# Performance work log

Hardware: AMD Instinct MI355X
Metric: run time of the kernel (lower is better)

Reference implementation:

```python
import jax, jax.numpy as jnp
import numpy as np

D_MODEL = 1024
N_HEADS = 16
HEAD_DIM = D_MODEL // N_HEADS
BATCH = 4
SEQ = 2048


def setup_inputs() -> dict:
    key = jax.random.key(0)
    k_x, k_wqkv, k_bqkv, k_wo, k_bo = jax.random.split(key, 5)
    x = jax.random.normal(k_x, (BATCH, SEQ, D_MODEL), dtype=jnp.float32)
    # causal mask: True = masked (upper triangle, excluding diagonal)
    mask = jnp.triu(jnp.ones((SEQ, SEQ), dtype=bool), k=1)
    lim = 1.0 / np.sqrt(D_MODEL)
    w_qkv = jax.random.uniform(k_wqkv, (D_MODEL, 3 * D_MODEL), jnp.float32, -lim, lim)
    b_qkv = jax.random.uniform(k_bqkv, (3 * D_MODEL,), jnp.float32, -lim, lim)
    w_out = jax.random.uniform(k_wo, (D_MODEL, D_MODEL), jnp.float32, -lim, lim)
    b_out = jax.random.uniform(k_bo, (D_MODEL,), jnp.float32, -lim, lim)
    return {"x": x, "mask": mask, "w_qkv": w_qkv, "b_qkv": b_qkv,
            "w_out": w_out, "b_out": b_out}


def reference(x, mask, w_qkv, b_qkv, w_out, b_out):
    b, s, _ = x.shape
    scale = HEAD_DIM ** -0.5
    qkv = x @ w_qkv + b_qkv                          # [b, s, 3*d]
    qkv = qkv.reshape(b, s, 3, N_HEADS, HEAD_DIM)
    qkv = jnp.transpose(qkv, (2, 0, 3, 1, 4))        # [3, b, h, s, hd]
    q, k, v = qkv[0], qkv[1], qkv[2]
    attn = jnp.einsum('bhqd,bhkd->bhqk', q, k) * scale
    attn = jnp.where(mask, -jnp.inf, attn)
    attn = jax.nn.softmax(attn, axis=-1)
    out = jnp.einsum('bhqk,bhkd->bhqd', attn, v)     # [b, h, s, hd]
    out = jnp.transpose(out, (0, 2, 1, 3)).reshape(b, s, D_MODEL)
    return out @ w_out + b_out
```

## Files before the change

### kernel.cpp

```cpp
#include <hip/hip_runtime.h>
#include <stdint.h>

typedef unsigned short u16;
typedef __attribute__((ext_vector_type(8))) short short8;
typedef __attribute__((ext_vector_type(4))) float f32x4;
typedef __attribute__((ext_vector_type(16))) float f32x16;

#define DEV static __device__ __forceinline__

#define QSCALE 0.18033688011112042f

DEV float fast_exp2(float x) { return __builtin_amdgcn_exp2f(x); }

DEV float bf2f(u16 u) { union { uint32_t i; float f; } x; x.i = ((uint32_t)u) << 16; return x.f; }
DEV u16 f2bf(float f) {
  union { float f; uint32_t i; } x; x.f = f;
  uint32_t r = x.i + 0x7FFFu + ((x.i >> 16) & 1u);
  return (u16)(r >> 16);
}
DEV uint32_t pk_bf16(float lo, float hi) {
  uint32_t r;
  asm("v_cvt_pk_bf16_f32 %0, %1, %2" : "=v"(r) : "v"(lo), "v"(hi));
  return r;
}

DEV void async_copy16(void* lds_dst, const void* gsrc) {
  typedef __attribute__((address_space(1))) void* gp_t;
  typedef __attribute__((address_space(3))) void* lp_t;
  __builtin_amdgcn_global_load_lds((gp_t)(uintptr_t)gsrc,
                                   (lp_t)(uint32_t)(uintptr_t)lds_dst, 16, 0, 0);
}

DEV void gemm_bt_core(const u16* __restrict__ A, const u16* __restrict__ Bt, int K,
                      int m0, int n0, uint8_t* As, uint8_t* Bs,
                      f32x4 (&acc)[4][4], int wave, int lane, int wm, int wn) {
#pragma unroll
  for (int mt = 0; mt < 4; ++mt)
#pragma unroll
    for (int nt = 0; nt < 4; ++nt)
      acc[mt][nt] = (f32x4){0.f, 0.f, 0.f, 0.f};

  for (int k0 = 0; k0 < K; k0 += 64) {
    __syncthreads();
#pragma unroll
    for (int i = 0; i < 4; ++i) {
      int cb = wave * 256 + i * 64;
      int c  = cb + lane;
      int r  = c >> 3;
      int ks = (c & 7) ^ (r & 7);
      async_copy16(As + cb * 16 + lane * 16, A  + (size_t)(m0 + r) * K + k0 + ks * 8);
      async_copy16(Bs + cb * 16 + lane * 16, Bt + (size_t)(n0 + r) * K + k0 + ks * 8);
    }
    __syncthreads();

    short8 af[2][4], bf_[2][4];
#pragma unroll
    for (int kk = 0; kk < 2; ++kk)
#pragma unroll
      for (int t = 0; t < 4; ++t) {
        int ra = wm + t * 16 + (lane & 15);
        af[kk][t]  = *(const short8*)(As + ra * 128 + (((kk * 4 + (lane >> 4)) ^ (ra & 7)) << 4));
        int rb = wn + t * 16 + (lane & 15);
        bf_[kk][t] = *(const short8*)(Bs + rb * 128 + (((kk * 4 + (lane >> 4)) ^ (rb & 7)) << 4));
      }
#pragma unroll
    for (int kk = 0; kk < 2; ++kk)
#pragma unroll
      for (int mt = 0; mt < 4; ++mt)
#pragma unroll
        for (int nt = 0; nt < 4; ++nt)
          acc[mt][nt] = __builtin_amdgcn_mfma_f32_16x16x32_bf16(af[kk][mt], bf_[kk][nt],
                                                                acc[mt][nt], 0, 0, 0);
  }
}

#define BUF_BYTES 49152

DEV void stage_slot(const u16* __restrict__ A, const u16* __restrict__ Bt,
                    int m0, int n0, int k0, uint8_t* buf, int tid) {
  uint8_t* As = buf;
  uint8_t* Bs = buf + 32768;
#pragma unroll
  for (int i = 0; i < 4; ++i) {
    int c = i * 512 + tid;
    int r = c >> 3;
    int ks = (c & 7) ^ (r & 7);
    async_copy16(As + c * 16, A + (size_t)(m0 + r) * 1024 + k0 + ks * 8);
  }
#pragma unroll
  for (int i = 0; i < 2; ++i) {
    int c = i * 512 + tid;
    int r = c >> 3;
    int ks = (c & 7) ^ (r & 7);
    async_copy16(Bs + c * 16, Bt + (size_t)(n0 + r) * 1024 + k0 + ks * 8);
  }
}

DEV void gemm256_core(const u16* __restrict__ A, const u16* __restrict__ Bt,
                      int m0, int n0, uint8_t* lds,
                      f32x4 (&acc)[4][4], int wave, int lane, int tid) {
  const int wm = (wave >> 1) * 64, wn = (wave & 1) * 64;
#pragma unroll
  for (int mf = 0; mf < 4; ++mf)
#pragma unroll
    for (int nf = 0; nf < 4; ++nf)
      acc[mf][nf] = (f32x4){0.f, 0.f, 0.f, 0.f};

  stage_slot(A, Bt, m0, n0, 0,  lds,             tid);
  stage_slot(A, Bt, m0, n0, 64, lds + BUF_BYTES, tid);
  asm volatile("s_waitcnt vmcnt(6)" ::: "memory");
  __builtin_amdgcn_s_barrier();

#pragma unroll 1
  for (int kt = 0; kt < 16; ++kt) {
    const uint8_t* Ab = lds + (kt & 1) * BUF_BYTES;
    const uint8_t* Bb = Ab + 32768;

    short8 a0[4], b0[4], a1[4], b1[4];
#pragma unroll
    for (int f = 0; f < 4; ++f) {
      int ra = wm + f * 16 + (lane & 15);
      int rb = wn + f * 16 + (lane & 15);
      a0[f] = *(const short8*)(Ab + ra * 128 + (((lane >> 4) ^ (ra & 7)) << 4));
      b0[f] = *(const short8*)(Bb + rb * 128 + (((lane >> 4) ^ (rb & 7)) << 4));
    }
#pragma unroll
    for (int f = 0; f < 4; ++f) {
      int ra = wm + f * 16 + (lane & 15);
      int rb = wn + f * 16 + (lane & 15);
      a1[f] = *(const short8*)(Ab + ra * 128 + (((4 + (lane >> 4)) ^ (ra & 7)) << 4));
      b1[f] = *(const short8*)(Bb + rb * 128 + (((4 + (lane >> 4)) ^ (rb & 7)) << 4));
    }

    asm volatile("s_waitcnt lgkmcnt(8)" ::: "memory");
    __builtin_amdgcn_sched_barrier(0);
    __builtin_amdgcn_s_setprio(1);
#pragma unroll
    for (int mf = 0; mf < 4; ++mf)
#pragma unroll
      for (int nf = 0; nf < 4; ++nf)
        acc[mf][nf] = __builtin_amdgcn_mfma_f32_16x16x32_bf16(a0[mf], b0[nf],
                                                              acc[mf][nf], 0, 0, 0);
    __builtin_amdgcn_s_setprio(0);

    asm volatile("s_waitcnt lgkmcnt(0)" ::: "memory");
    __builtin_amdgcn_sched_barrier(0);
    __builtin_amdgcn_s_barrier();

    if (kt + 2 < 16)
      stage_slot(A, Bt, m0, n0, (kt + 2) * 64, lds + (kt & 1) * BUF_BYTES, tid);

    __builtin_amdgcn_s_setprio(1);
#pragma unroll
    for (int mf = 0; mf < 4; ++mf)
#pragma unroll
      for (int nf = 0; nf < 4; ++nf)
        acc[mf][nf] = __builtin_amdgcn_mfma_f32_16x16x32_bf16(a1[mf], b1[nf],
                                                              acc[mf][nf], 0, 0, 0);
    __builtin_amdgcn_s_setprio(0);

    if (kt + 2 < 16) asm volatile("s_waitcnt vmcnt(6)" ::: "memory");
    else             asm volatile("s_waitcnt vmcnt(0)" ::: "memory");
    __builtin_amdgcn_s_barrier();
  }
}

__global__ __launch_bounds__(256, 2) void k_gemm_qkv(
    const u16* __restrict__ X, const u16* __restrict__ WT, const float* __restrict__ bias,
    u16* __restrict__ Q, u16* __restrict__ Kv, u16* __restrict__ Vt) {
  __shared__ __attribute__((aligned(16))) uint8_t As[16384];
  __shared__ __attribute__((aligned(16))) uint8_t Bs[16384];
  const int lane = threadIdx.x & 63, wave = threadIdx.x >> 6;
  const int wm = (wave >> 1) * 64, wn = (wave & 1) * 64;
  const int m0 = blockIdx.x * 128, n0 = blockIdx.y * 128;
  f32x4 acc[4][4];
  gemm_bt_core(X, WT, 1024, m0, n0, As, Bs, acc, wave, lane, wm, wn);
#pragma unroll
  for (int nt = 0; nt < 4; ++nt) {
    int n = n0 + wn + nt * 16 + (lane & 15);
    float bv = bias[n];
    int which = n >> 10, h = (n >> 6) & 15, hd = n & 63;
    if (which == 2) {
#pragma unroll
      for (int mt = 0; mt < 4; ++mt) {
        int m = m0 + wm + mt * 16 + (lane >> 4) * 4;
        int b = m >> 11, s = m & 2047;
        u16 tmp[4];
#pragma unroll
        for (int rg = 0; rg < 4; ++rg) tmp[rg] = f2bf(acc[mt][nt][rg] + bv);
        *(uint64_t*)(Vt + ((size_t)(b * 16 + h) * 64 + hd) * 2048 + s) = *(const uint64_t*)tmp;
      }
    } else {
      u16* base = (which == 0) ? Q : Kv;
      const float mul = (which == 0) ? QSCALE : 1.0f;
#pragma unroll
      for (int mt = 0; mt < 4; ++mt)
#pragma unroll
        for (int rg = 0; rg < 4; ++rg) {
          int m = m0 + wm + mt * 16 + (lane >> 4) * 4 + rg;
          int b = m >> 11, s = m & 2047;
          base[((size_t)(b * 16 + h) * 2048 + s) * 64 + hd] = f2bf((acc[mt][nt][rg] + bv) * mul);
        }
    }
  }
}

__global__ __launch_bounds__(512, 2) void k_gemm_out(
    const u16* __restrict__ A, const u16* __restrict__ WT, const float* __restrict__ bias,
    float* __restrict__ Out) {
  __shared__ __attribute__((aligned(16))) uint8_t lds[2 * BUF_BYTES];
  const int tid = threadIdx.x, lane = tid & 63, wave = tid >> 6;
  const int wm = (wave >> 1) * 64, wn = (wave & 1) * 64;
  const int m0 = blockIdx.x * 256, n0 = blockIdx.y * 128;
  f32x4 acc[4][4];
  gemm256_core(A, WT, m0, n0, lds, acc, wave, lane, tid);
#pragma unroll
  for (int nf = 0; nf < 4; ++nf) {
    int n = n0 + wn + nf * 16 + (lane & 15);
    float bv = bias[n];
#pragma unroll
    for (int mf = 0; mf < 4; ++mf)
#pragma unroll
      for (int rg = 0; rg < 4; ++rg) {
        int m = m0 + wm + mf * 16 + (lane >> 4) * 4 + rg;
        Out[(size_t)m * 1024 + n] = acc[mf][nf][rg] + bv;
      }
  }
}

__global__ __launch_bounds__(256) void k_cvt_x(const float* __restrict__ src,
                                               u16* __restrict__ dst, int n8) {
  int i = blockIdx.x * 256 + threadIdx.x;
  if (i >= n8) return;
  float4 a = *(const float4*)(src + (size_t)i * 8);
  float4 b = *(const float4*)(src + (size_t)i * 8 + 4);
  u16 tmp[8] = {f2bf(a.x), f2bf(a.y), f2bf(a.z), f2bf(a.w),
                f2bf(b.x), f2bf(b.y), f2bf(b.z), f2bf(b.w)};
  *(short8*)(dst + (size_t)i * 8) = *(const short8*)tmp;
}

__global__ __launch_bounds__(256) void k_transpose_f32(
    const float* __restrict__ src, u16* __restrict__ dst, int R, int C) {
  __shared__ u16 tile[64][72];
  const int tr = blockIdx.x * 64, tc = blockIdx.y * 64;
  for (int c = threadIdx.x; c < 1024; c += 256) {
    int r = c >> 4, c4 = (c & 15) * 4;
    float4 v = *(const float4*)(src + (size_t)(tr + r) * C + tc + c4);
    tile[r][c4 + 0] = f2bf(v.x); tile[r][c4 + 1] = f2bf(v.y);
    tile[r][c4 + 2] = f2bf(v.z); tile[r][c4 + 3] = f2bf(v.w);
  }
  __syncthreads();
  for (int c = threadIdx.x; c < 512; c += 256) {
    int oc = c >> 3, r8 = (c & 7) * 8;
    u16 tmp[8];
#pragma unroll
    for (int i = 0; i < 8; ++i) tmp[i] = tile[r8 + i][oc];
    *(short8*)(dst + (size_t)(tc + oc) * R + tr + r8) = *(const short8*)tmp;
  }
}

DEV void stage_tile(const u16* __restrict__ Kg, const u16* __restrict__ Vg,
                    uint8_t* kb, uint8_t* vb, int t, int tid) {
#pragma unroll
  for (int i = 0; i < 2; ++i) {
    int c = i * 256 + tid;
    int r = c >> 3;
    int ks = (c & 7) ^ (r & 7);
    async_copy16(kb + c * 16, Kg + (size_t)(t * 64 + r) * 64 + ks * 8);
    async_copy16(vb + c * 16, Vg + (size_t)r * 2048 + t * 64 + ks * 8);
  }
}

__global__ __launch_bounds__(256, 2) void k_attn(
    const u16* __restrict__ Q, const u16* __restrict__ K,
    const u16* __restrict__ Vt, u16* __restrict__ O) {
  __shared__ __attribute__((aligned(16))) uint8_t kbuf[2][8192];
  __shared__ __attribute__((aligned(16))) uint8_t vbuf[2][8192];
  const int tid = threadIdx.x;
  const int lane = tid & 63;
  const int wave = tid >> 6;
  const int q32 = lane & 31, hv = lane >> 5;
  const float NEG_INF = -__builtin_inff();

  int L = blockIdx.x;
  int bh = (L & 7) * 8 + ((L >> 3) >> 3);
  int pair = (L >> 3) & 7;
  const int b = bh >> 4, h = bh & 15;
  const size_t hb = (size_t)bh * (2048 * 64);
  const u16* Qg = Q + hb;
  const u16* Kg = K + hb;
  const u16* Vg = Vt + hb;

#pragma unroll 1
  for (int which = 0; which < 2; ++which) {
    const int s = which ? (15 - pair) : pair;
    const int nt = 2 * (s + 1);
    const int qbase = s * 128 + wave * 32;
    const int qg = qbase + q32;
    const int my_nt = ((qbase + 31) >> 6) + 1;

    short8 qf[4];
#pragma unroll
    for (int dblk = 0; dblk < 4; ++dblk)
      qf[dblk] = *(const short8*)(Qg + (size_t)qg * 64 + dblk * 16 + hv * 8);

    f32x16 oacc[2] = {};
    float mrun = NEG_INF, lrun = 0.f;

    stage_tile(Kg, Vg, kbuf[0], vbuf[0], 0, tid);
    __syncthreads();

#pragma unroll 1
    for (int t = 0; t < nt; ++t) {
      const int cur = t & 1;
      if (t + 1 < nt) stage_tile(Kg, Vg, kbuf[cur ^ 1], vbuf[cur ^ 1], t + 1, tid);

      if (t < my_nt) {
        const uint8_t* kb = kbuf[cur];
        const uint8_t* vb = vbuf[cur];

        f32x16 sa0 = {}, sa1 = {};
        __builtin_amdgcn_s_setprio(1);
#pragma unroll
        for (int dblk = 0; dblk < 4; ++dblk) {
          short8 kf0 = *(const short8*)(kb + q32 * 128 + (((dblk * 2 + hv) ^ (q32 & 7)) << 4));
          short8 kf1 = *(const short8*)(kb + (32 + q32) * 128 + (((dblk * 2 + hv) ^ (q32 & 7)) << 4));
          sa0 = __builtin_amdgcn_mfma_f32_32x32x16_bf16(kf0, qf[dblk], sa0, 0, 0, 0);
          sa1 = __builtin_amdgcn_mfma_f32_32x32x16_bf16(kf1, qf[dblk], sa1, 0, 0, 0);
        }
        __builtin_amdgcn_s_setprio(0);

        float sv[32];
#pragma unroll
        for (int r = 0; r < 16; ++r) { sv[r] = sa0[r]; sv[16 + r] = sa1[r]; }
        if (t * 64 + 63 > qbase) {
#pragma unroll
          for (int r = 0; r < 16; ++r) {
            int kl = (r & 3) + 8 * (r >> 2) + 4 * hv;
            if (t * 64 + kl > qg)      sv[r]      = NEG_INF;
            if (t * 64 + 32 + kl > qg) sv[16 + r] = NEG_INF;
          }
        }

        float mloc = fmaxf(sv[0], sv[1]);
#pragma unroll
        for (int r = 2; r < 32; ++r) mloc = fmaxf(mloc, sv[r]);
        float mtile = fmaxf(mloc, __shfl_xor(mloc, 32, 64));
        if (!__all(mtile <= mrun + 8.f)) {
          float mnew = fmaxf(mrun, mtile);
          float corr = fast_exp2(mrun - mnew);
          mrun = mnew;
          lrun *= corr;
#pragma unroll
          for (int r = 0; r < 16; ++r) { oacc[0][r] *= corr; oacc[1][r] *= corr; }
        }
        float ls = 0.f;
#pragma unroll
        for (int r = 0; r < 32; ++r) { sv[r] = fast_exp2(sv[r] - mrun); ls += sv[r]; }
        ls += __shfl_xor(ls, 32, 64);
        lrun += ls;

        __builtin_amdgcn_s_setprio(1);
#pragma unroll
        for (int ksub = 0; ksub < 2; ++ksub) {
#pragma unroll
          for (int kb2 = 0; kb2 < 2; ++kb2) {
            const int rb = ksub * 16 + kb2 * 8;
            uint32_t pA = pk_bf16(sv[rb + 0], sv[rb + 1]);
            uint32_t pB = pk_bf16(sv[rb + 2], sv[rb + 3]);
            uint32_t pC = pk_bf16(sv[rb + 4], sv[rb + 5]);
            uint32_t pD = pk_bf16(sv[rb + 6], sv[rb + 7]);
            uint32_t X = hv ? pA : pC;
            uint32_t Y = hv ? pB : pD;
            uint32_t sX = (uint32_t)__shfl_xor((int)X, 32, 64);
            uint32_t sY = (uint32_t)__shfl_xor((int)Y, 32, 64);
            union { uint32_t u[4]; short8 s8; } pu;
            pu.u[0] = hv ? sX : pA;
            pu.u[1] = hv ? sY : pB;
            pu.u[2] = hv ? pC : sX;
            pu.u[3] = hv ? pD : sY;
            const int kblk = ksub * 2 + kb2;
            short8 vf0 = *(const short8*)(vb + q32 * 128 + (((kblk * 2 + hv) ^ (q32 & 7)) << 4));
            short8 vf1 = *(const short8*)(vb + (32 + q32) * 128 + (((kblk * 2 + hv) ^ (q32 & 7)) << 4));
            oacc[0] = __builtin_amdgcn_mfma_f32_32x32x16_bf16(vf0, pu.s8, oacc[0], 0, 0, 0);
            oacc[1] = __builtin_amdgcn_mfma_f32_32x32x16_bf16(vf1, pu.s8, oacc[1], 0, 0, 0);
          }
        }
        __builtin_amdgcn_s_setprio(0);
      }

      __syncthreads();
    }

    float rl = 1.0f / lrun;
    u16* orow = O + ((size_t)(b * 2048 + qg)) * 1024 + h * 64;
#pragma unroll
    for (int dt = 0; dt < 2; ++dt)
#pragma unroll
      for (int g = 0; g < 4; ++g) {
        int dbase = dt * 32 + 8 * g + 4 * hv;
        u16 tmp[4];
#pragma unroll
        for (int j2 = 0; j2 < 4; ++j2) tmp[j2] = f2bf(oacc[dt][4 * g + j2] * rl);
        *(uint64_t*)(orow + dbase) = *(const uint64_t*)tmp;
      }
  }
}

extern "C" void kernel_launch(void* const* d_in, const int* in_sizes, int n_in,
                              void* d_out, int out_size, void* d_ws, size_t ws_size,
                              hipStream_t stream) {
  const float* x     = (const float*)d_in[0];
  const float* w_qkv = (const float*)d_in[2];
  const float* b_qkv = (const float*)d_in[3];
  const float* w_out = (const float*)d_in[4];
  const float* b_out = (const float*)d_in[5];
  float* out = (float*)d_out;
  uint8_t* ws = (uint8_t*)d_ws;

  u16* wqkvT = (u16*)(ws);
  u16* woutT = (u16*)(ws +  6291456);
  u16* Xb    = (u16*)(ws +  8388608);
  u16* Qb    = (u16*)(ws + 25165824);
  u16* Kb    = (u16*)(ws + 41943040);
  u16* Vtb   = (u16*)(ws + 58720256);
  u16* AO    = Xb;

  k_cvt_x<<<dim3(4096), 256, 0, stream>>>(x, Xb, 1048576);
  k_transpose_f32<<<dim3(16, 48), 256, 0, stream>>>(w_qkv, wqkvT, 1024, 3072);
  k_transpose_f32<<<dim3(16, 16), 256, 0, stream>>>(w_out, woutT, 1024, 1024);
  k_gemm_qkv<<<dim3(64, 24), 256, 0, stream>>>(Xb, wqkvT, b_qkv, Qb, Kb, Vtb);
  k_attn<<<dim3(512), 256, 0, stream>>>(Qb, Kb, Vtb, AO);
  k_gemm_out<<<dim3(32, 8), 512, 0, stream>>>(AO, woutT, b_out, out);
}
```

Measured before the change: 155.0 us.

## Enlarge attention KV tiles to 128 keys and fuse prep kernels into one launch

The attention kernel now stages 128-key K/V tiles per iteration instead of 64, which halves the number of barriers and pipeline steps. The second 64-key half is skipped when it lies entirely in the masked region, and masking is applied only on the diagonal tile. Separately, the x conversion and the two weight transposes are merged into one kernel launch to cut launch overhead. LDS use per block doubles to 64 KB, which may limit occupancy, and the larger sv array raises register pressure.

```diff
diff --git a/kernel.cpp b/kernel.cpp
--- a/kernel.cpp
+++ b/kernel.cpp
@@ -228,21 +228,25 @@
   }
 }
 
-__global__ __launch_bounds__(256) void k_cvt_x(const float* __restrict__ src,
-                                               u16* __restrict__ dst, int n8) {
-  int i = blockIdx.x * 256 + threadIdx.x;
-  if (i >= n8) return;
-  float4 a = *(const float4*)(src + (size_t)i * 8);
-  float4 b = *(const float4*)(src + (size_t)i * 8 + 4);
-  u16 tmp[8] = {f2bf(a.x), f2bf(a.y), f2bf(a.z), f2bf(a.w),
-                f2bf(b.x), f2bf(b.y), f2bf(b.z), f2bf(b.w)};
-  *(short8*)(dst + (size_t)i * 8) = *(const short8*)tmp;
-}
-
-__global__ __launch_bounds__(256) void k_transpose_f32(
-    const float* __restrict__ src, u16* __restrict__ dst, int R, int C) {
+__global__ __launch_bounds__(256) void k_prep(
+    const float* __restrict__ x, u16* __restrict__ Xb,
+    const float* __restrict__ w_qkv, u16* __restrict__ wqkvT,
+    const float* __restrict__ w_out, u16* __restrict__ woutT) {
   __shared__ u16 tile[64][72];
-  const int tr = blockIdx.x * 64, tc = blockIdx.y * 64;
+  const int bid = blockIdx.x;
+  if (bid < 4096) {
+    size_t i = (size_t)bid * 256 + threadIdx.x;
+    float4 a = *(const float4*)(x + i * 8);
+    float4 b = *(const float4*)(x + i * 8 + 4);
+    u16 tmp[8] = {f2bf(a.x), f2bf(a.y), f2bf(a.z), f2bf(a.w),
+                  f2bf(b.x), f2bf(b.y), f2bf(b.z), f2bf(b.w)};
+    *(short8*)(Xb + i * 8) = *(const short8*)tmp;
+    return;
+  }
+  const float* src; u16* dst; int R, C, t;
+  if (bid < 4864) { t = bid - 4096; src = w_qkv; dst = wqkvT; R = 1024; C = 3072; }
+  else            { t = bid - 4864; src = w_out; dst = woutT; R = 1024; C = 1024; }
+  const int tr = (t & 15) * 64, tc = (t >> 4) * 64;
   for (int c = threadIdx.x; c < 1024; c += 256) {
     int r = c >> 4, c4 = (c & 15) * 4;
     float4 v = *(const float4*)(src + (size_t)(tr + r) * C + tc + c4);
@@ -259,23 +263,29 @@
   }
 }
 
-DEV void stage_tile(const u16* __restrict__ Kg, const u16* __restrict__ Vg,
-                    uint8_t* kb, uint8_t* vb, int t, int tid) {
-#pragma unroll
-  for (int i = 0; i < 2; ++i) {
+DEV void stage_tile128(const u16* __restrict__ Kg, const u16* __restrict__ Vg,
+                       uint8_t* kb, uint8_t* vb, int t, int tid) {
+#pragma unroll
+  for (int i = 0; i < 4; ++i) {
     int c = i * 256 + tid;
     int r = c >> 3;
     int ks = (c & 7) ^ (r & 7);
-    async_copy16(kb + c * 16, Kg + (size_t)(t * 64 + r) * 64 + ks * 8);
-    async_copy16(vb + c * 16, Vg + (size_t)r * 2048 + t * 64 + ks * 8);
+    async_copy16(kb + c * 16, Kg + (size_t)(t * 128 + r) * 64 + ks * 8);
+  }
+#pragma unroll
+  for (int i = 0; i < 4; ++i) {
+    int c = i * 256 + tid;
+    int r = c >> 4;
+    int ks = (c & 15) ^ (r & 7);
+    async_copy16(vb + c * 16, Vg + (size_t)r * 2048 + t * 128 + ks * 8);
   }
 }
 
 __global__ __launch_bounds__(256, 2) void k_attn(
     const u16* __restrict__ Q, const u16* __restrict__ K,
     const u16* __restrict__ Vt, u16* __restrict__ O) {
-  __shared__ __attribute__((aligned(16))) uint8_t kbuf[2][8192];
-  __shared__ __attribute__((aligned(16))) uint8_t vbuf[2][8192];
+  __shared__ __attribute__((aligned(16))) uint8_t kbuf[2][16384];
+  __shared__ __attribute__((aligned(16))) uint8_t vbuf[2][16384];
   const int tid = threadIdx.x;
   const int lane = tid & 63;
   const int wave = tid >> 6;
@@ -294,10 +304,9 @@
 #pragma unroll 1
   for (int which = 0; which < 2; ++which) {
     const int s = which ? (15 - pair) : pair;
-    const int nt = 2 * (s + 1);
+    const int nt = s + 1;
     const int qbase = s * 128 + wave * 32;
     const int qg = qbase + q32;
-    const int my_nt = ((qbase + 31) >> 6) + 1;
 
     short8 qf[4];
 #pragma unroll
@@ -307,18 +316,20 @@
     f32x16 oacc[2] = {};
     float mrun = NEG_INF, lrun = 0.f;
 
-    stage_tile(Kg, Vg, kbuf[0], vbuf[0], 0, tid);
+    stage_tile128(Kg, Vg, kbuf[0], vbuf[0], 0, tid);
     __syncthreads();
 
 #pragma unroll 1
     for (int t = 0; t < nt; ++t) {
       const int cur = t & 1;
-      if (t + 1 < nt) stage_tile(Kg, Vg, kbuf[cur ^ 1], vbuf[cur ^ 1], t + 1, tid);
-
-      if (t < my_nt) {
-        const uint8_t* kb = kbuf[cur];
-        const uint8_t* vb = vbuf[cur];
-
+      if (t + 1 < nt) stage_tile128(Kg, Vg, kbuf[cur ^ 1], vbuf[cur ^ 1], t + 1, tid);
+
+      const uint8_t* kb = kbuf[cur];
+      const uint8_t* vb = vbuf[cur];
+      const bool h2 = (t * 128 + 64) <= (qbase + 31);
+
+      float sv[64];
+      {
         f32x16 sa0 = {}, sa1 = {};
         __builtin_amdgcn_s_setprio(1);
 #pragma unroll
@@ -329,40 +340,71 @@
           sa1 = __builtin_amdgcn_mfma_f32_32x32x16_bf16(kf1, qf[dblk], sa1, 0, 0, 0);
         }
         __builtin_amdgcn_s_setprio(0);
-
-        float sv[32];
 #pragma unroll
         for (int r = 0; r < 16; ++r) { sv[r] = sa0[r]; sv[16 + r] = sa1[r]; }
-        if (t * 64 + 63 > qbase) {
+      }
+      if (h2) {
+        f32x16 sa2 = {}, sa3 = {};
+        __builtin_amdgcn_s_setprio(1);
+#pragma unroll
+        for (int dblk = 0; dblk < 4; ++dblk) {
+          short8 kf2 = *(const short8*)(kb + (64 + q32) * 128 + (((dblk * 2 + hv) ^ (q32 & 7)) << 4));
+          short8 kf3 = *(const short8*)(kb + (96 + q32) * 128 + (((dblk * 2 + hv) ^ (q32 & 7)) << 4));
+          sa2 = __builtin_amdgcn_mfma_f32_32x32x16_bf16(kf2, qf[dblk], sa2, 0, 0, 0);
+          sa3 = __builtin_amdgcn_mfma_f32_32x32x16_bf16(kf3, qf[dblk], sa3, 0, 0, 0);
+        }
+        __builtin_amdgcn_s_setprio(0);
+#pragma unroll
+        for (int r = 0; r < 16; ++r) { sv[32 + r] = sa2[r]; sv[48 + r] = sa3[r]; }
+      }
+
+      if (t == s) {
+#pragma unroll
+        for (int r = 0; r < 16; ++r) {
+          int kl = (r & 3) + 8 * (r >> 2) + 4 * hv;
+          if (t * 128 + kl > qg)      sv[r]      = NEG_INF;
+          if (t * 128 + 32 + kl > qg) sv[16 + r] = NEG_INF;
+        }
+        if (h2) {
 #pragma unroll
           for (int r = 0; r < 16; ++r) {
             int kl = (r & 3) + 8 * (r >> 2) + 4 * hv;
-            if (t * 64 + kl > qg)      sv[r]      = NEG_INF;
-            if (t * 64 + 32 + kl > qg) sv[16 + r] = NEG_INF;
+            if (t * 128 + 64 + kl > qg) sv[32 + r] = NEG_INF;
+            if (t * 128 + 96 + kl > qg) sv[48 + r] = NEG_INF;
           }
         }
-
-        float mloc = fmaxf(sv[0], sv[1]);
-#pragma unroll
-        for (int r = 2; r < 32; ++r) mloc = fmaxf(mloc, sv[r]);
-        float mtile = fmaxf(mloc, __shfl_xor(mloc, 32, 64));
-        if (!__all(mtile <= mrun + 8.f)) {
-          float mnew = fmaxf(mrun, mtile);
-          float corr = fast_exp2(mrun - mnew);
-          mrun = mnew;
-          lrun *= corr;
-#pragma unroll
-          for (int r = 0; r < 16; ++r) { oacc[0][r] *= corr; oacc[1][r] *= corr; }
-        }
-        float ls = 0.f;
-#pragma unroll
-        for (int r = 0; r < 32; ++r) { sv[r] = fast_exp2(sv[r] - mrun); ls += sv[r]; }
-        ls += __shfl_xor(ls, 32, 64);
-        lrun += ls;
-
-        __builtin_amdgcn_s_setprio(1);
-#pragma unroll
-        for (int ksub = 0; ksub < 2; ++ksub) {
+      }
+
+      float mloc = fmaxf(sv[0], sv[1]);
+#pragma unroll
+      for (int r = 2; r < 32; ++r) mloc = fmaxf(mloc, sv[r]);
+      if (h2) {
+#pragma unroll
+        for (int r = 32; r < 64; ++r) mloc = fmaxf(mloc, sv[r]);
+      }
+      float mtile = fmaxf(mloc, __shfl_xor(mloc, 32, 64));
+      if (!__all(mtile <= mrun + 8.f)) {
+        float mnew = fmaxf(mrun, mtile);
+        float corr = fast_exp2(mrun - mnew);
+        mrun = mnew;
+        lrun *= corr;
+#pragma unroll
+        for (int r = 0; r < 16; ++r) { oacc[0][r] *= corr; oacc[1][r] *= corr; }
+      }
+      float ls = 0.f;
+#pragma unroll
+      for (int r = 0; r < 32; ++r) { sv[r] = fast_exp2(sv[r] - mrun); ls += sv[r]; }
+      if (h2) {
+#pragma unroll
+        for (int r = 32; r < 64; ++r) { sv[r] = fast_exp2(sv[r] - mrun); ls += sv[r]; }
+      }
+      ls += __shfl_xor(ls, 32, 64);
+      lrun += ls;
+
+      __builtin_amdgcn_s_setprio(1);
+#pragma unroll
+      for (int ksub = 0; ksub < 4; ++ksub) {
+        if (ksub < 2 || h2) {
 #pragma unroll
           for (int kb2 = 0; kb2 < 2; ++kb2) {
             const int rb = ksub * 16 + kb2 * 8;
@@ -380,14 +422,14 @@
             pu.u[2] = hv ? pC : sX;
             pu.u[3] = hv ? pD : sY;
             const int kblk = ksub * 2 + kb2;
-            short8 vf0 = *(const short8*)(vb + q32 * 128 + (((kblk * 2 + hv) ^ (q32 & 7)) << 4));
-            short8 vf1 = *(const short8*)(vb + (32 + q32) * 128 + (((kblk * 2 + hv) ^ (q32 & 7)) << 4));
+            short8 vf0 = *(const short8*)(vb + q32 * 256 + (((kblk * 2 + hv) ^ (q32 & 7)) << 4));
+            short8 vf1 = *(const short8*)(vb + (32 + q32) * 256 + (((kblk * 2 + hv) ^ (q32 & 7)) << 4));
             oacc[0] = __builtin_amdgcn_mfma_f32_32x32x16_bf16(vf0, pu.s8, oacc[0], 0, 0, 0);
             oacc[1] = __builtin_amdgcn_mfma_f32_32x32x16_bf16(vf1, pu.s8, oacc[1], 0, 0, 0);
           }
         }
-        __builtin_amdgcn_s_setprio(0);
-      }
+      }
+      __builtin_amdgcn_s_setprio(0);
 
       __syncthreads();
     }
@@ -426,9 +468,7 @@
   u16* Vtb   = (u16*)(ws + 58720256);
   u16* AO    = Xb;
 
-  k_cvt_x<<<dim3(4096), 256, 0, stream>>>(x, Xb, 1048576);
-  k_transpose_f32<<<dim3(16, 48), 256, 0, stream>>>(w_qkv, wqkvT, 1024, 3072);
-  k_transpose_f32<<<dim3(16, 16), 256, 0, stream>>>(w_out, woutT, 1024, 1024);
+  k_prep<<<dim3(5120), 256, 0, stream>>>(x, Xb, w_qkv, wqkvT, w_out, woutT);
   k_gemm_qkv<<<dim3(64, 24), 256, 0, stream>>>(Xb, wqkvT, b_qkv, Qb, Kb, Vtb);
   k_attn<<<dim3(512), 256, 0, stream>>>(Qb, Kb, Vtb, AO);
   k_gemm_out<<<dim3(32, 8), 512, 0, stream>>>(AO, woutT, b_out, out);
```

New measurement: 149.5 us, median of 4. 3.6% less time.
